# Kernel tuning notes

Hardware: AMD Instinct MI355X
Metric: run time of the kernel (lower is better)

The kernel has to match this reference:

```python
import jax, jax.numpy as jnp
import numpy as np

B, H, W, DIM, NH = 2, 48, 48, 768, 12
HD = DIM // NH  # 64


def setup_inputs() -> dict:
    key = jax.random.key(0)
    ks = jax.random.split(key, 7)
    std = 0.02
    return {
        "x": jax.random.normal(ks[0], (B, H, W, DIM), jnp.float32),
        "rel_pos_h": jax.random.normal(ks[1], (2 * H - 1, HD), jnp.float32) * std,
        "rel_pos_w": jax.random.normal(ks[2], (2 * W - 1, HD), jnp.float32) * std,
        "qkv_w": jax.random.normal(ks[3], (3 * DIM, DIM), jnp.float32) * std,
        "qkv_b": jnp.zeros((3 * DIM,), jnp.float32),
        "proj_w": jax.random.normal(ks[4], (DIM, DIM), jnp.float32) * std,
        "proj_b": jnp.zeros((DIM,), jnp.float32),
    }


def reference(x, rel_pos_h, rel_pos_w, qkv_w, qkv_b, proj_w, proj_b):
    b, h, w, dim = x.shape
    nh = NH
    hd = dim // nh
    scale = hd ** -0.5
    n = h * w
    # qkv projection: (B,N,3*dim) -> (3, B*nh, N, hd)
    qkv = x.reshape(b, n, dim) @ qkv_w.T + qkv_b
    qkv = qkv.reshape(b, n, 3, nh, hd).transpose(2, 0, 3, 1, 4).reshape(3, b * nh, n, hd)
    q, k, v = qkv[0], qkv[1], qkv[2]
    # scaled dot-product scores (B*nh, N, N)
    attn = jnp.einsum('bnc,bmc->bnm', q * scale, k)
    # decomposed relative position bias (q_size == k_size, no interpolation)
    idx_h = jnp.arange(h)[:, None] - jnp.arange(h)[None, :] + (h - 1)  # (h,h)
    idx_w = jnp.arange(w)[:, None] - jnp.arange(w)[None, :] + (w - 1)  # (w,w)
    Rh = rel_pos_h[idx_h]  # (h, h, hd)
    Rw = rel_pos_w[idx_w]  # (w, w, hd)
    r_q = q.reshape(b * nh, h, w, hd)
    rel_h = jnp.einsum('bhwc,hkc->bhwk', r_q, Rh)  # (B*nh, h, w, h)
    rel_w = jnp.einsum('bhwc,wkc->bhwk', r_q, Rw)  # (B*nh, h, w, w)
    attn = (attn.reshape(b * nh, h, w, h, w)
            + rel_h[:, :, :, :, None]
            + rel_w[:, :, :, None, :]).reshape(b * nh, n, n)
    attn = jax.nn.softmax(attn, axis=-1)
    out = (attn @ v).reshape(b, nh, h, w, hd).transpose(0, 2, 3, 1, 4).reshape(b, h, w, dim)
    return out @ proj_w.T + proj_b
```

## Files before the change

### kernel.cpp

```cpp
#include <hip/hip_runtime.h>
#include <hip/hip_bf16.h>
#include <stdint.h>

#define NQ    2304
#define MROWS 4608
#define DIMC  768
#define NHEAD 12
#define HEADS 24
#define HD    64

typedef unsigned int uint;
typedef unsigned short u16;
typedef __attribute__((ext_vector_type(8))) short s16x8;
typedef __attribute__((ext_vector_type(4))) float f32x4;

#define MFMA16(a, b, c) __builtin_amdgcn_mfma_f32_16x16x32_bf16((a), (b), (c), 0, 0, 0)

static __device__ __forceinline__ float bfbits2f(uint u) {
  union { uint i; float f; } c; c.i = u << 16; return c.f;
}
static __device__ __forceinline__ u16 f2bf(float f) {
  __hip_bfloat16 h = __float2bfloat16(f);
  union { __hip_bfloat16 h; u16 u; } c; c.h = h; return c.u;
}
static __device__ __forceinline__ u16 f2h(float f) {
  union { _Float16 h; u16 u; } c; c.h = (_Float16)f; return c.u;
}
static __device__ __forceinline__ float h2f(u16 u) {
  union { u16 u; _Float16 h; } c; c.u = u; return (float)c.h;
}
static __device__ __forceinline__ void dec8(uint4 p, float* f) {
  f[0] = bfbits2f(p.x & 0xFFFFu); f[1] = bfbits2f(p.x >> 16);
  f[2] = bfbits2f(p.y & 0xFFFFu); f[3] = bfbits2f(p.y >> 16);
  f[4] = bfbits2f(p.z & 0xFFFFu); f[5] = bfbits2f(p.z >> 16);
  f[6] = bfbits2f(p.w & 0xFFFFu); f[7] = bfbits2f(p.w >> 16);
}
static __device__ __forceinline__ void ld8(const void* p, size_t idx, int bf, float* f) {
  if (bf) { dec8(*(const uint4*)((const u16*)p + idx), f); }
  else {
    const float4* q = (const float4*)((const float*)p + idx);
    float4 a = q[0], b = q[1];
    f[0] = a.x; f[1] = a.y; f[2] = a.z; f[3] = a.w;
    f[4] = b.x; f[5] = b.y; f[6] = b.z; f[7] = b.w;
  }
}
static __device__ __forceinline__ float ld1(const void* p, size_t idx, int bf) {
  return bf ? bfbits2f(((const u16*)p)[idx]) : ((const float*)p)[idx];
}
static __device__ __forceinline__ uint4 ld8_to_bf(const void* p, size_t idx, int bf) {
  if (bf) return *(const uint4*)((const u16*)p + idx);
  float f[8]; ld8(p, idx, 0, f);
  uint4 u;
  u.x = (uint)f2bf(f[0]) | ((uint)f2bf(f[1]) << 16);
  u.y = (uint)f2bf(f[2]) | ((uint)f2bf(f[3]) << 16);
  u.z = (uint)f2bf(f[4]) | ((uint)f2bf(f[5]) << 16);
  u.w = (uint)f2bf(f[6]) | ((uint)f2bf(f[7]) << 16);
  return u;
}
static __device__ __forceinline__ void gll16(const u16* g, u16* l) {
  __builtin_amdgcn_global_load_lds(
      (const __attribute__((address_space(1))) unsigned int*)g,
      (__attribute__((address_space(3))) unsigned int*)l, 16, 0, 0);
}

__global__ __launch_bounds__(256) void detect_k(const u16* __restrict__ x,
                                                int* __restrict__ mode) {
  __shared__ int wsum[4];
  int t = threadIdx.x;
  int cnt = 0;
  for (int i = 0; i < 8; ++i) {
    uint u = x[(size_t)(t * 8 + i) * 2];
    uint e = (u >> 7) & 0xFFu;
    uint mag = u & 0x7FFFu;
    if (mag == 0 || (e >= 113 && e <= 133)) cnt++;
  }
#pragma unroll
  for (int d = 1; d < 64; d <<= 1) cnt += __shfl_xor(cnt, d);
  if ((t & 63) == 0) wsum[t >> 6] = cnt;
  __syncthreads();
  if (t == 0) mode[0] = ((wsum[0] + wsum[1] + wsum[2] + wsum[3]) > 1024) ? 1 : 0;
}

#define NX8 442368u
#define NW8 221184u
#define NP8 73728u
__global__ __launch_bounds__(256) void convert_k(
    const void* __restrict__ x, const void* __restrict__ qkvw,
    const void* __restrict__ pw, const int* __restrict__ mode,
    u16* __restrict__ xb, u16* __restrict__ wb, u16* __restrict__ pwb)
{
  const int bf = mode[0];
  uint i8 = blockIdx.x * 256 + threadIdx.x;
  if (i8 < NX8) {
    *(uint4*)(xb + (size_t)i8 * 8) = ld8_to_bf(x, (size_t)i8 * 8, bf);
  } else if (i8 < NX8 + NW8) {
    size_t j = i8 - NX8;
    *(uint4*)(wb + j * 8) = ld8_to_bf(qkvw, j * 8, bf);
  } else if (i8 < NX8 + NW8 + NP8) {
    size_t j = i8 - NX8 - NW8;
    *(uint4*)(pwb + j * 8) = ld8_to_bf(pw, j * 8, bf);
  }
}

__global__ __launch_bounds__(256) void qkv_gemm_k(
    const u16* __restrict__ Xb, const u16* __restrict__ Wb,
    const void* __restrict__ Bq, const int* __restrict__ mode,
    u16* __restrict__ Q, u16* __restrict__ K, u16* __restrict__ V)
{
  __shared__ __align__(16) u16 As[128][32];
  __shared__ __align__(16) u16 Bs[128][32];
  const int bf = mode[0];
  const int t = threadIdx.x;
  const int w = t >> 6, lane = t & 63, l15 = t & 15, quad = (t >> 4) & 3;
  const int wr = w >> 1, wc = w & 1;
  const int row0 = blockIdx.y << 7, col0 = blockIdx.x << 7;
  const int r4 = lane >> 2, c8 = (lane & 3) << 3;

  f32x4 zero4 = {0.f, 0.f, 0.f, 0.f};
  f32x4 acc[4][4];
#pragma unroll
  for (int i = 0; i < 4; ++i)
#pragma unroll
    for (int j = 0; j < 4; ++j) acc[i][j] = zero4;

  for (int kt = 0; kt < DIMC; kt += 32) {
    __syncthreads();
    gll16(Xb + (size_t)(row0 + (w << 5) + r4) * DIMC + kt + c8,      &As[(w << 5)][0]);
    gll16(Xb + (size_t)(row0 + (w << 5) + 16 + r4) * DIMC + kt + c8, &As[(w << 5) + 16][0]);
    gll16(Wb + (size_t)(col0 + (w << 5) + r4) * DIMC + kt + c8,      &Bs[(w << 5)][0]);
    gll16(Wb + (size_t)(col0 + (w << 5) + 16 + r4) * DIMC + kt + c8, &Bs[(w << 5) + 16][0]);
    __syncthreads();
    s16x8 af[4], bfr[4];
#pragma unroll
    for (int i = 0; i < 4; ++i)
      af[i] = *(const s16x8*)&As[(wr << 6) + (i << 4) + l15][quad << 3];
#pragma unroll
    for (int j = 0; j < 4; ++j)
      bfr[j] = *(const s16x8*)&Bs[(wc << 6) + (j << 4) + l15][quad << 3];
#pragma unroll
    for (int i = 0; i < 4; ++i)
#pragma unroll
      for (int j = 0; j < 4; ++j)
        acc[i][j] = MFMA16(af[i], bfr[j], acc[i][j]);
  }

#pragma unroll
  for (int jt = 0; jt < 4; ++jt) {
    int col = col0 + (wc << 6) + (jt << 4) + l15;
    int which = col / DIMC;
    int rem = col - which * DIMC;
    int head = rem >> 6, d = rem & 63;
    float bv = ld1(Bq, col, bf);
    u16* dst = (which == 0) ? Q : (which == 1) ? K : V;
#pragma unroll
    for (int i = 0; i < 4; ++i)
#pragma unroll
      for (int r = 0; r < 4; ++r) {
        int mrow = row0 + (wr << 6) + (i << 4) + (quad << 2) + r;
        int b_ = (mrow >= NQ) ? 1 : 0;
        int n = mrow - b_ * NQ;
        dst[(((size_t)(b_ * NHEAD + head)) * NQ + n) * HD + d] = f2bf(acc[i][jt][r] + bv);
      }
  }
}

__global__ __launch_bounds__(256) void vtrans_k(
    const u16* __restrict__ V, u16* __restrict__ Vt)
{
  __shared__ __align__(16) u16 L[64][72];
  const int blk = blockIdx.x;
  const int bhd = blk / 36;
  const int n0 = (blk - bhd * 36) << 6;
  const int t = threadIdx.x;
  const int r = t >> 3, c8 = (t & 7) << 3;

  const u16* src = V + ((size_t)bhd * NQ + n0) * HD;
  *(uint4*)&L[r][c8]      = *(const uint4*)(src + (size_t)r * HD + c8);
  *(uint4*)&L[r + 32][c8] = *(const uint4*)(src + (size_t)(r + 32) * HD + c8);
  __syncthreads();

  u16* dst = Vt + (size_t)bhd * HD * NQ + n0;
#pragma unroll
  for (int half = 0; half < 2; ++half) {
    int d = r + (half << 5);
    u16 tmp[8];
#pragma unroll
    for (int j = 0; j < 8; ++j) tmp[j] = L[c8 + j][d];
    *(uint4*)(dst + (size_t)d * NQ + c8) = *(uint4*)tmp;
  }
}

__global__ __launch_bounds__(256) void bias_gemm_k(
    const u16* __restrict__ Qw,
    const void* __restrict__ rph, const void* __restrict__ rpw,
    const int* __restrict__ mode,
    u16* __restrict__ Bh_g, u16* __restrict__ Bw_g)
{
  __shared__ __align__(16) u16 As[128][72];
  __shared__ __align__(16) u16 Bs[192][72];
  const int bf = mode[0];
  const int t = threadIdx.x;
  const int w = t >> 6, l15 = t & 15, quad = (t >> 4) & 3;
  const int wr = w >> 1, wc = w & 1;
  const int blk = blockIdx.x;
  const int bhd = blk / 18;
  const int row0 = (blk - bhd * 18) << 7;

  {
    int lr = t >> 1, lk = (t & 1) << 5;
    const u16* src = Qw + ((size_t)bhd * NQ + row0 + lr) * HD + lk;
    *(uint4*)&As[lr][lk]      = *(const uint4*)(src);
    *(uint4*)&As[lr][lk + 8]  = *(const uint4*)(src + 8);
    *(uint4*)&As[lr][lk + 16] = *(const uint4*)(src + 16);
    *(uint4*)&As[lr][lk + 24] = *(const uint4*)(src + 24);
  }
  for (int e = t; e < 384; e += 256) {
    int row = e >> 1, k32 = (e & 1) << 5;
    int tab = (row >= 96) ? 1 : 0;
    int r2 = row - (tab ? 96 : 0);
    if (r2 > 94) r2 = 0;
    const void* src = tab ? rpw : rph;
    *(uint4*)&Bs[row][k32]      = ld8_to_bf(src, (size_t)r2 * HD + k32, bf);
    *(uint4*)&Bs[row][k32 + 8]  = ld8_to_bf(src, (size_t)r2 * HD + k32 + 8, bf);
    *(uint4*)&Bs[row][k32 + 16] = ld8_to_bf(src, (size_t)r2 * HD + k32 + 16, bf);
    *(uint4*)&Bs[row][k32 + 24] = ld8_to_bf(src, (size_t)r2 * HD + k32 + 24, bf);
  }
  __syncthreads();

  f32x4 zero4 = {0.f, 0.f, 0.f, 0.f};
  f32x4 acc[4][6];
#pragma unroll
  for (int i = 0; i < 4; ++i)
#pragma unroll
    for (int j = 0; j < 6; ++j) acc[i][j] = zero4;

#pragma unroll
  for (int ks = 0; ks < 2; ++ks) {
    s16x8 af[4], bfr[6];
#pragma unroll
    for (int i = 0; i < 4; ++i)
      af[i] = *(const s16x8*)&As[(wr << 6) + (i << 4) + l15][(ks << 5) + (quad << 3)];
#pragma unroll
    for (int j = 0; j < 6; ++j)
      bfr[j] = *(const s16x8*)&Bs[wc * 96 + (j << 4) + l15][(ks << 5) + (quad << 3)];
#pragma unroll
    for (int i = 0; i < 4; ++i)
#pragma unroll
      for (int j = 0; j < 6; ++j)
        acc[i][j] = MFMA16(af[i], bfr[j], acc[i][j]);
  }

#pragma unroll
  for (int jt = 0; jt < 6; ++jt) {
    int col = wc * 96 + (jt << 4) + l15;
    int tab = (col >= 96) ? 1 : 0;
    int j = col - (tab ? 96 : 0);
    if (j >= 95) continue;
    u16* dstT = tab ? Bw_g : Bh_g;
#pragma unroll
    for (int i = 0; i < 4; ++i)
#pragma unroll
      for (int r = 0; r < 4; ++r) {
        int n = row0 + (wr << 6) + (i << 4) + (quad << 2) + r;
        int qh = (n * 10923) >> 19;
        int coord = tab ? (n - qh * 48) : qh;
        int c = coord + 47 - j;
        if (c >= 0 && c < 48)
          dstT[((size_t)bhd * 48 + c) * NQ + n] = f2h(acc[i][jt][r]);
      }
  }
}

#define ATILE(KB, KN, T0, PREF, KM) do {                                      \
    f32x4 acc_s[2][4];                                                        \
    _Pragma("unroll")                                                         \
    for (int nc = 0; nc < 4; ++nc) {                                          \
      f32x4 a0 = MFMA16(KB[2*nc], qa0[0], zero4);                             \
      acc_s[0][nc] = MFMA16(KB[2*nc+1], qa1[0], a0);                          \
      f32x4 a1 = MFMA16(KB[2*nc], qa0[1], zero4);                             \
      acc_s[1][nc] = MFMA16(KB[2*nc+1], qa1[1], a1);                          \
    }                                                                         \
    if (PREF) {                                                               \
      _Pragma("unroll")                                                       \
      for (int nc = 0; nc < 4; ++nc) {                                        \
        const u16* kp_ = kbase + (size_t)((T0) + 64 + (nc << 4) + l15) * HD + (quad << 3); \
        KN[2*nc]   = *(const s16x8*)(kp_);                                    \
        KN[2*nc+1] = *(const s16x8*)(kp_ + 32);                               \
      }                                                                       \
    }                                                                         \
    int kh0 = ((T0) * 10923) >> 19;                                           \
    int thr = (kh0 + 1) * 48 - (T0);                                          \
    uint Wq[2][8];                                                            \
    _Pragma("unroll")                                                         \
    for (int g = 0; g < 2; ++g) {                                             \
      int qrl = (w << 5) + (g << 4) + l15;                                    \
      float bh0v = h2f(BhL[kh0][qrl]);                                        \
      float bh1v = h2f(BhL[kh0 + 1][qrl]);                                    \
      float sum = 0.f;                                                        \
      _Pragma("unroll")                                                       \
      for (int nc = 0; nc < 4; ++nc) {                                        \
        int bnc = (KM) + (nc << 4);                                           \
        bnc = (bnc >= 48) ? bnc - 48 : bnc;                                   \
        uint2 pv = *(const uint2*)&BwL[qrl][bnc + (quad << 2)];               \
        float b0 = h2f((u16)(pv.x & 0xFFFFu));                                \
        float b1 = h2f((u16)(pv.x >> 16));                                    \
        float b2 = h2f((u16)(pv.y & 0xFFFFu));                                \
        float b3 = h2f((u16)(pv.y >> 16));                                    \
        int kl = (nc << 4) + (quad << 2);                                     \
        float e0 = __expf(acc_s[g][nc][0] * scale + ((kl     >= thr) ? bh1v : bh0v) + b0); \
        float e1 = __expf(acc_s[g][nc][1] * scale + ((kl + 1 >= thr) ? bh1v : bh0v) + b1); \
        float e2 = __expf(acc_s[g][nc][2] * scale + ((kl + 2 >= thr) ? bh1v : bh0v) + b2); \
        float e3 = __expf(acc_s[g][nc][3] * scale + ((kl + 3 >= thr) ? bh1v : bh0v) + b3); \
        sum += (e0 + e1) + (e2 + e3);                                         \
        Wq[g][2*nc]   = (uint)f2bf(e0) | ((uint)f2bf(e1) << 16);              \
        Wq[g][2*nc+1] = (uint)f2bf(e2) | ((uint)f2bf(e3) << 16);              \
      }                                                                       \
      l_st[g] += sum;                                                         \
    }                                                                         \
    _Pragma("unroll")                                                         \
    for (int h = 0; h < 2; ++h) {                                             \
      s16x8 vb[4];                                                            \
      _Pragma("unroll")                                                       \
      for (int nc = 0; nc < 4; ++nc)                                          \
        vb[nc] = *(const s16x8*)(vtbase + (size_t)((nc << 4) + l15) * NQ      \
                                 + (T0) + (h << 5) + (quad << 3));            \
      _Pragma("unroll")                                                       \
      for (int g = 0; g < 2; ++g) {                                           \
        uint e0 = __shfl(Wq[g][4*h+0], srcA), e1 = __shfl(Wq[g][4*h+1], srcA); \
        uint e2 = __shfl(Wq[g][4*h+2], srcA), e3 = __shfl(Wq[g][4*h+3], srcA); \
        uint g0 = __shfl(Wq[g][4*h+0], srcB), g1 = __shfl(Wq[g][4*h+1], srcB); \
        uint g2 = __shfl(Wq[g][4*h+2], srcB), g3 = __shfl(Wq[g][4*h+3], srcB); \
        union { uint u[4]; s16x8 v; } pf;                                     \
        pf.u[0] = hi ? e2 : e0; pf.u[1] = hi ? e3 : e1;                       \
        pf.u[2] = hi ? g2 : g0; pf.u[3] = hi ? g3 : g1;                       \
        _Pragma("unroll")                                                     \
        for (int nc = 0; nc < 4; ++nc)                                        \
          acc_o[g][nc] = MFMA16(pf.v, vb[nc], acc_o[g][nc]);                  \
      }                                                                       \
    }                                                                         \
  } while (0)

__global__ __launch_bounds__(256) void attn_k(
    const u16* __restrict__ Qw, const u16* __restrict__ Kw,
    const u16* __restrict__ Vtg,
    const u16* __restrict__ Bh_g, const u16* __restrict__ Bw_g,
    int S, float* __restrict__ Opart, float* __restrict__ Lpart,
    u16* __restrict__ Aout)
{
  __shared__ __align__(16) u16 BhL[48][128];
  __shared__ __align__(16) u16 BwL[128][52];

  const int bid = blockIdx.x;
  const int xcd = bid & 7;
  const int local = bid >> 3;
  const int per_head = 18 * S;
  const int head_l = local / per_head;
  const int rem = local - head_l * per_head;
  const int qb = rem / S;
  const int z = rem - qb * S;
  const int bhd = xcd * 3 + head_l;
  const int q0 = qb << 7;
  const int span = NQ / S;
  const int kt_lo = z * span, kt_hi = kt_lo + span;

  const int t = threadIdx.x;
  const int w = t >> 6, l15 = t & 15, quad = (t >> 4) & 3;
  const float scale = 0.125f;

  const u16* kbase  = Kw  + (size_t)bhd * NQ * HD;
  const u16* vtbase = Vtg + (size_t)bhd * HD * NQ;
  const int q0w = q0 + (w << 5);

  for (int e = t; e < 768; e += 256) {
    int c = e >> 4;
    int off = (e & 15) << 3;
    size_t gi = ((size_t)bhd * 48 + c) * NQ + q0 + off;
    *(uint4*)&BhL[c][off] = *(const uint4*)(Bh_g + gi);
    uint4 wv = *(const uint4*)(Bw_g + gi);
    u16 vals[8];
    vals[0] = wv.x & 0xFFFFu; vals[1] = wv.x >> 16;
    vals[2] = wv.y & 0xFFFFu; vals[3] = wv.y >> 16;
    vals[4] = wv.z & 0xFFFFu; vals[5] = wv.z >> 16;
    vals[6] = wv.w & 0xFFFFu; vals[7] = wv.w >> 16;
#pragma unroll
    for (int j = 0; j < 8; ++j) BwL[off + j][c] = vals[j];
  }

  s16x8 qa0[2], qa1[2];
#pragma unroll
  for (int g = 0; g < 2; ++g) {
    const u16* qfrag = Qw + ((size_t)bhd * NQ + q0w + (g << 4) + l15) * HD + (quad << 3);
    qa0[g] = *(const s16x8*)(qfrag);
    qa1[g] = *(const s16x8*)(qfrag + 32);
  }

  s16x8 kbA[8], kbB[8];
#pragma unroll
  for (int nc = 0; nc < 4; ++nc) {
    const u16* kp = kbase + (size_t)(kt_lo + (nc << 4) + l15) * HD + (quad << 3);
    kbA[2*nc]   = *(const s16x8*)(kp);
    kbA[2*nc+1] = *(const s16x8*)(kp + 32);
  }

  __syncthreads();

  f32x4 zero4 = {0.f, 0.f, 0.f, 0.f};
  f32x4 acc_o[2][4];
#pragma unroll
  for (int g = 0; g < 2; ++g)
#pragma unroll
    for (int nc = 0; nc < 4; ++nc) acc_o[g][nc] = zero4;
  float l_st[2] = {0.f, 0.f};
  const int srcA = ((quad & 1) << 5) + l15;
  const int srcB = srcA + 16;
  const int hi = quad >> 1;
  int km = 0;

  for (int kt0 = kt_lo; kt0 < kt_hi; kt0 += 128) {
    ATILE(kbA, kbB, kt0, 1, km);
    km += 16; if (km >= 48) km -= 48;
    int pref2 = (kt0 + 128) < kt_hi;
    ATILE(kbB, kbA, kt0 + 64, pref2, km);
    km += 16; if (km >= 48) km -= 48;
  }

#pragma unroll
  for (int g = 0; g < 2; ++g) {
    float lg = l_st[g];
    lg += __shfl_xor(lg, 16);
    lg += __shfl_xor(lg, 32);
    if (S > 1) {
      float* Op = Opart + ((size_t)(z * HEADS + bhd) * NQ + q0) * HD;
#pragma unroll
      for (int r = 0; r < 4; ++r) {
        int row = (w << 5) + (g << 4) + (quad << 2) + r;
#pragma unroll
        for (int nc = 0; nc < 4; ++nc)
          Op[(size_t)row * HD + (nc << 4) + l15] = acc_o[g][nc][r];
      }
      if (quad == 0)
        Lpart[(size_t)(z * HEADS + bhd) * NQ + q0w + (g << 4) + l15] = lg;
    } else {
      int b_ = bhd / NHEAD, head = bhd - b_ * NHEAD;
      float invl = 1.f / lg;
      int bsrc = (quad << 4) + (quad << 2);
#pragma unroll
      for (int r = 0; r < 4; ++r) {
        float inv = __shfl(invl, bsrc + r);
        int token = q0 + (w << 5) + (g << 4) + (quad << 2) + r;
        u16* dst = Aout + ((size_t)b_ * NQ + token) * DIMC + (head << 6);
#pragma unroll
        for (int nc = 0; nc < 4; ++nc)
          dst[(nc << 4) + l15] = f2bf(acc_o[g][nc][r] * inv);
      }
    }
  }
}

__global__ __launch_bounds__(256) void combine_k(
    const float* __restrict__ Op, const float* __restrict__ Lp,
    int S, u16* __restrict__ Aout)
{
  int idx = blockIdx.x * 256 + threadIdx.x;
  int m = idx / 192;
  int cq = idx - m * 192;
  int ccol = cq << 2;
  int head = ccol >> 6, d0 = ccol & 63;
  int b_ = (m >= NQ) ? 1 : 0;
  int n = m - b_ * NQ;
  int bh = b_ * NHEAD + head;
  float ox = 0.f, oy = 0.f, oz = 0.f, ow = 0.f, ls = 0.f;
  for (int zz = 0; zz < S; ++zz) {
    const float* ob = Op + ((size_t)(zz * HEADS + bh) * NQ + n) * HD + d0;
    float4 v = *(const float4*)ob;
    ox += v.x; oy += v.y; oz += v.z; ow += v.w;
    ls += Lp[(size_t)(zz * HEADS + bh) * NQ + n];
  }
  float inv = 1.f / ls;
  u16* dst = Aout + (size_t)m * DIMC + ccol;
  dst[0] = f2bf(ox * inv); dst[1] = f2bf(oy * inv);
  dst[2] = f2bf(oz * inv); dst[3] = f2bf(ow * inv);
}

__global__ __launch_bounds__(256) void proj_gemm_k(
    const u16* __restrict__ A, const u16* __restrict__ Wb,
    const void* __restrict__ Bp, const int* __restrict__ mode,
    void* __restrict__ Out)
{
  __shared__ __align__(16) u16 As[128][32];
  __shared__ __align__(16) u16 Bs[128][32];
  const int bf = mode[0];
  const int t = threadIdx.x;
  const int w = t >> 6, lane = t & 63, l15 = t & 15, quad = (t >> 4) & 3;
  const int wr = w >> 1, wc = w & 1;
  const int row0 = blockIdx.y << 7, col0 = blockIdx.x << 7;
  const int r4 = lane >> 2, c8 = (lane & 3) << 3;

  f32x4 zero4 = {0.f, 0.f, 0.f, 0.f};
  f32x4 acc[4][4];
#pragma unroll
  for (int i = 0; i < 4; ++i)
#pragma unroll
    for (int j = 0; j < 4; ++j) acc[i][j] = zero4;

  for (int kt = 0; kt < DIMC; kt += 32) {
    __syncthreads();
    gll16(A + (size_t)(row0 + (w << 5) + r4) * DIMC + kt + c8,       &As[(w << 5)][0]);
    gll16(A + (size_t)(row0 + (w << 5) + 16 + r4) * DIMC + kt + c8,  &As[(w << 5) + 16][0]);
    gll16(Wb + (size_t)(col0 + (w << 5) + r4) * DIMC + kt + c8,      &Bs[(w << 5)][0]);
    gll16(Wb + (size_t)(col0 + (w << 5) + 16 + r4) * DIMC + kt + c8, &Bs[(w << 5) + 16][0]);
    __syncthreads();
    s16x8 af[4], bfr[4];
#pragma unroll
    for (int i = 0; i < 4; ++i)
      af[i] = *(const s16x8*)&As[(wr << 6) + (i << 4) + l15][quad << 3];
#pragma unroll
    for (int j = 0; j < 4; ++j)
      bfr[j] = *(const s16x8*)&Bs[(wc << 6) + (j << 4) + l15][quad << 3];
#pragma unroll
    for (int i = 0; i < 4; ++i)
#pragma unroll
      for (int j = 0; j < 4; ++j)
        acc[i][j] = MFMA16(af[i], bfr[j], acc[i][j]);
  }

#pragma unroll
  for (int jt = 0; jt < 4; ++jt) {
    int col = col0 + (wc << 6) + (jt << 4) + l15;
    float bv = ld1(Bp, col, bf);
#pragma unroll
    for (int i = 0; i < 4; ++i)
#pragma unroll
      for (int r = 0; r < 4; ++r) {
        int mrow = row0 + (wr << 6) + (i << 4) + (quad << 2) + r;
        float val = acc[i][jt][r] + bv;
        size_t off = (size_t)mrow * DIMC + col;
        if (bf) ((u16*)Out)[off] = f2bf(val);
        else    ((float*)Out)[off] = val;
      }
  }
}

extern "C" void kernel_launch(void* const* d_in, const int* in_sizes, int n_in,
                              void* d_out, int out_size, void* d_ws, size_t ws_size,
                              hipStream_t stream)
{
  const void* x    = d_in[0];
  const void* rph  = d_in[1];
  const void* rpw  = d_in[2];
  const void* qkvw = d_in[3];
  const void* qkvb = d_in[4];
  const void* pw   = d_in[5];
  const void* pb   = d_in[6];

  int* mode = (int*)d_ws;
  const size_t qkv_elems = (size_t)HEADS * NQ * HD;
  const size_t NXe = (size_t)MROWS * DIMC;
  const size_t NWe = (size_t)3 * DIMC * DIMC;
  const size_t NPe = (size_t)DIMC * DIMC;
  u16* q    = (u16*)((char*)d_ws + 16);
  u16* k    = q + qkv_elems;
  u16* vt   = k + qkv_elems;
  u16* aout = vt + qkv_elems;
  u16* v    = aout;
  u16* pwb  = aout + qkv_elems;
  const size_t biasElems = (size_t)HEADS * 48 * NQ;
  u16* bh_g = pwb + NPe;
  u16* bw_g = bh_g + biasElems;
  char* R   = (char*)(bw_g + biasElems);
  const size_t baseR = (size_t)((char*)R - (char*)d_ws);
  u16* xb = (u16*)R;
  u16* wb = xb + NXe;
  const size_t needXW = (NXe + NWe) * 2;
  const size_t perO = (size_t)HEADS * NQ * HD * 4;
  const size_t perL = (size_t)HEADS * NQ * 4;

  int S = 1;
  size_t n3 = 3 * (perO + perL), n2 = 2 * (perO + perL);
  if (ws_size >= baseR + (n3 > needXW ? n3 : needXW)) S = 3;
  else if (ws_size >= baseR + (n2 > needXW ? n2 : needXW)) S = 2;
  float* opart = (float*)R;
  float* lpart = (float*)(R + (size_t)S * perO);

  detect_k<<<1, 256, 0, stream>>>((const u16*)x, mode);
  convert_k<<<dim3(2880), 256, 0, stream>>>(x, qkvw, pw, mode, xb, wb, pwb);
  qkv_gemm_k<<<dim3(18, 36), 256, 0, stream>>>(xb, wb, qkvb, mode, q, k, v);
  vtrans_k<<<dim3(864), 256, 0, stream>>>(v, vt);
  bias_gemm_k<<<dim3(432), 256, 0, stream>>>(q, rph, rpw, mode, bh_g, bw_g);
  attn_k<<<dim3(432 * S), 256, 0, stream>>>(q, k, vt, bh_g, bw_g,
                                            S, opart, lpart, aout);
  if (S > 1)
    combine_k<<<dim3(3456), 256, 0, stream>>>(opart, lpart, S, aout);
  proj_gemm_k<<<dim3(6, 36), 256, 0, stream>>>(aout, pwb, pb, mode, d_out);
}
```

Before: 335.4 us.

## Fuse V transpose into QKV GEMM epilogue, use exp2 softmax, add MFMA priority hints

The QKV GEMM epilogue now transposes the V tile through shared memory and writes Vt directly. This removes the separate vtrans kernel launch and the V round trip through global memory. Softmax now uses exp2, with log2e folded into the stored bias tables and the score scale. s_setprio hints are placed around the MFMA blocks in the attention tile. The fused epilogue adds an extra LDS buffer and barriers to the V-column GEMM blocks.

Result: no change. 341.0 us (+1.7%).

```diff
diff --git a/kernel.cpp b/kernel.cpp
--- a/kernel.cpp
+++ b/kernel.cpp
@@ -15,6 +15,7 @@
 typedef __attribute__((ext_vector_type(4))) float f32x4;
 
 #define MFMA16(a, b, c) __builtin_amdgcn_mfma_f32_16x16x32_bf16((a), (b), (c), 0, 0, 0)
+#define LOG2E 1.44269504f
 
 static __device__ __forceinline__ float bfbits2f(uint u) {
   union { uint i; float f; } c; c.i = u << 16; return c.f;
@@ -28,6 +29,13 @@
 }
 static __device__ __forceinline__ float h2f(u16 u) {
   union { u16 u; _Float16 h; } c; c.u = u; return (float)c.h;
+}
+static __device__ __forceinline__ float fexp2(float x) {
+#if __has_builtin(__builtin_amdgcn_exp2f)
+  return __builtin_amdgcn_exp2f(x);
+#else
+  return __expf(x * 0.69314718f);
+#endif
 }
 static __device__ __forceinline__ void dec8(uint4 p, float* f) {
   f[0] = bfbits2f(p.x & 0xFFFFu); f[1] = bfbits2f(p.x >> 16);
@@ -105,10 +113,11 @@
 __global__ __launch_bounds__(256) void qkv_gemm_k(
     const u16* __restrict__ Xb, const u16* __restrict__ Wb,
     const void* __restrict__ Bq, const int* __restrict__ mode,
-    u16* __restrict__ Q, u16* __restrict__ K, u16* __restrict__ V)
+    u16* __restrict__ Q, u16* __restrict__ K, u16* __restrict__ Vt)
 {
   __shared__ __align__(16) u16 As[128][32];
   __shared__ __align__(16) u16 Bs[128][32];
+  __shared__ __align__(16) u16 Ts[128][72];
   const int bf = mode[0];
   const int t = threadIdx.x;
   const int w = t >> 6, lane = t & 63, l15 = t & 15, quad = (t >> 4) & 3;
@@ -144,49 +153,57 @@
         acc[i][j] = MFMA16(af[i], bfr[j], acc[i][j]);
   }
 
-#pragma unroll
-  for (int jt = 0; jt < 4; ++jt) {
-    int col = col0 + (wc << 6) + (jt << 4) + l15;
-    int which = col / DIMC;
-    int rem = col - which * DIMC;
-    int head = rem >> 6, d = rem & 63;
-    float bv = ld1(Bq, col, bf);
-    u16* dst = (which == 0) ? Q : (which == 1) ? K : V;
-#pragma unroll
-    for (int i = 0; i < 4; ++i)
-#pragma unroll
-      for (int r = 0; r < 4; ++r) {
-        int mrow = row0 + (wr << 6) + (i << 4) + (quad << 2) + r;
-        int b_ = (mrow >= NQ) ? 1 : 0;
-        int n = mrow - b_ * NQ;
-        dst[(((size_t)(b_ * NHEAD + head)) * NQ + n) * HD + d] = f2bf(acc[i][jt][r] + bv);
+  if (blockIdx.x < 12) {
+#pragma unroll
+    for (int jt = 0; jt < 4; ++jt) {
+      int col = col0 + (wc << 6) + (jt << 4) + l15;
+      int which = col / DIMC;
+      int rem = col - which * DIMC;
+      int head = rem >> 6, d = rem & 63;
+      float bv = ld1(Bq, col, bf);
+      u16* dst = (which == 0) ? Q : K;
+#pragma unroll
+      for (int i = 0; i < 4; ++i)
+#pragma unroll
+        for (int r = 0; r < 4; ++r) {
+          int mrow = row0 + (wr << 6) + (i << 4) + (quad << 2) + r;
+          int b_ = (mrow >= NQ) ? 1 : 0;
+          int n = mrow - b_ * NQ;
+          dst[(((size_t)(b_ * NHEAD + head)) * NQ + n) * HD + d] = f2bf(acc[i][jt][r] + bv);
+        }
+    }
+  } else {
+    int b_ = (row0 >= NQ) ? 1 : 0;
+    int n0 = row0 - b_ * NQ;
+#pragma unroll
+    for (int h = 0; h < 2; ++h) {
+      if (wc == h) {
+#pragma unroll
+        for (int jt = 0; jt < 4; ++jt) {
+          int coll = (jt << 4) + l15;
+          float bv = ld1(Bq, col0 + (h << 6) + coll, bf);
+#pragma unroll
+          for (int i = 0; i < 4; ++i)
+#pragma unroll
+            for (int r = 0; r < 4; ++r) {
+              int tok = (wr << 6) + (i << 4) + (quad << 2) + r;
+              Ts[tok][coll] = f2bf(acc[i][jt][r] + bv);
+            }
+        }
       }
-  }
-}
-
-__global__ __launch_bounds__(256) void vtrans_k(
-    const u16* __restrict__ V, u16* __restrict__ Vt)
-{
-  __shared__ __align__(16) u16 L[64][72];
-  const int blk = blockIdx.x;
-  const int bhd = blk / 36;
-  const int n0 = (blk - bhd * 36) << 6;
-  const int t = threadIdx.x;
-  const int r = t >> 3, c8 = (t & 7) << 3;
-
-  const u16* src = V + ((size_t)bhd * NQ + n0) * HD;
-  *(uint4*)&L[r][c8]      = *(const uint4*)(src + (size_t)r * HD + c8);
-  *(uint4*)&L[r + 32][c8] = *(const uint4*)(src + (size_t)(r + 32) * HD + c8);
-  __syncthreads();
-
-  u16* dst = Vt + (size_t)bhd * HD * NQ + n0;
-#pragma unroll
-  for (int half = 0; half < 2; ++half) {
-    int d = r + (half << 5);
-    u16 tmp[8];
-#pragma unroll
-    for (int j = 0; j < 8; ++j) tmp[j] = L[c8 + j][d];
-    *(uint4*)(dst + (size_t)d * NQ + c8) = *(uint4*)tmp;
+      __syncthreads();
+      int head = ((col0 - 1536) >> 6) + h;
+      u16* dst = Vt + ((size_t)(b_ * NHEAD + head) * HD) * NQ + n0;
+      int d = t >> 2, ch = (t & 3) << 5;
+#pragma unroll
+      for (int c4 = 0; c4 < 4; ++c4) {
+        u16 tmp[8];
+#pragma unroll
+        for (int j = 0; j < 8; ++j) tmp[j] = Ts[ch + (c4 << 3) + j][d];
+        *(uint4*)(dst + (size_t)d * NQ + ch + (c4 << 3)) = *(uint4*)tmp;
+      }
+      __syncthreads();
+    }
   }
 }
 
@@ -266,13 +283,14 @@
         int coord = tab ? (n - qh * 48) : qh;
         int c = coord + 47 - j;
         if (c >= 0 && c < 48)
-          dstT[((size_t)bhd * 48 + c) * NQ + n] = f2h(acc[i][jt][r]);
+          dstT[((size_t)bhd * 48 + c) * NQ + n] = f2h(acc[i][jt][r] * LOG2E);
       }
   }
 }
 
 #define ATILE(KB, KN, T0, PREF, KM) do {                                      \
     f32x4 acc_s[2][4];                                                        \
+    __builtin_amdgcn_s_setprio(1);                                            \
     _Pragma("unroll")                                                         \
     for (int nc = 0; nc < 4; ++nc) {                                          \
       f32x4 a0 = MFMA16(KB[2*nc], qa0[0], zero4);                             \
@@ -280,6 +298,7 @@
       f32x4 a1 = MFMA16(KB[2*nc], qa0[1], zero4);                             \
       acc_s[1][nc] = MFMA16(KB[2*nc+1], qa1[1], a1);                          \
     }                                                                         \
+    __builtin_amdgcn_s_setprio(0);                                            \
     if (PREF) {                                                               \
       _Pragma("unroll")                                                       \
       for (int nc = 0; nc < 4; ++nc) {                                        \
@@ -307,10 +326,10 @@
         float b2 = h2f((u16)(pv.y & 0xFFFFu));                                \
         float b3 = h2f((u16)(pv.y >> 16));                                    \
         int kl = (nc << 4) + (quad << 2);                                     \
-        float e0 = __expf(acc_s[g][nc][0] * scale + ((kl     >= thr) ? bh1v : bh0v) + b0); \
-        float e1 = __expf(acc_s[g][nc][1] * scale + ((kl + 1 >= thr) ? bh1v : bh0v) + b1); \
-        float e2 = __expf(acc_s[g][nc][2] * scale + ((kl + 2 >= thr) ? bh1v : bh0v) + b2); \
-        float e3 = __expf(acc_s[g][nc][3] * scale + ((kl + 3 >= thr) ? bh1v : bh0v) + b3); \
+        float e0 = fexp2(fmaf(acc_s[g][nc][0], scl2, ((kl     >= thr) ? bh1v : bh0v)) + b0); \
+        float e1 = fexp2(fmaf(acc_s[g][nc][1], scl2, ((kl + 1 >= thr) ? bh1v : bh0v)) + b1); \
+        float e2 = fexp2(fmaf(acc_s[g][nc][2], scl2, ((kl + 2 >= thr) ? bh1v : bh0v)) + b2); \
+        float e3 = fexp2(fmaf(acc_s[g][nc][3], scl2, ((kl + 3 >= thr) ? bh1v : bh0v)) + b3); \
         sum += (e0 + e1) + (e2 + e3);                                         \
         Wq[g][2*nc]   = (uint)f2bf(e0) | ((uint)f2bf(e1) << 16);              \
         Wq[g][2*nc+1] = (uint)f2bf(e2) | ((uint)f2bf(e3) << 16);              \
@@ -333,9 +352,11 @@
         union { uint u[4]; s16x8 v; } pf;                                     \
         pf.u[0] = hi ? e2 : e0; pf.u[1] = hi ? e3 : e1;                       \
         pf.u[2] = hi ? g2 : g0; pf.u[3] = hi ? g3 : g1;                       \
+        __builtin_amdgcn_s_setprio(1);                                        \
         _Pragma("unroll")                                                     \
         for (int nc = 0; nc < 4; ++nc)                                        \
           acc_o[g][nc] = MFMA16(pf.v, vb[nc], acc_o[g][nc]);                  \
+        __builtin_amdgcn_s_setprio(0);                                        \
       }                                                                       \
     }                                                                         \
   } while (0)
@@ -365,7 +386,7 @@
 
   const int t = threadIdx.x;
   const int w = t >> 6, l15 = t & 15, quad = (t >> 4) & 3;
-  const float scale = 0.125f;
+  const float scl2 = 0.125f * LOG2E;
 
   const u16* kbase  = Kw  + (size_t)bhd * NQ * HD;
   const u16* vtbase = Vtg + (size_t)bhd * HD * NQ;
@@ -562,7 +583,6 @@
   u16* k    = q + qkv_elems;
   u16* vt   = k + qkv_elems;
   u16* aout = vt + qkv_elems;
-  u16* v    = aout;
   u16* pwb  = aout + qkv_elems;
   const size_t biasElems = (size_t)HEADS * 48 * NQ;
   u16* bh_g = pwb + NPe;
@@ -584,8 +604,7 @@
 
   detect_k<<<1, 256, 0, stream>>>((const u16*)x, mode);
   convert_k<<<dim3(2880), 256, 0, stream>>>(x, qkvw, pw, mode, xb, wb, pwb);
-  qkv_gemm_k<<<dim3(18, 36), 256, 0, stream>>>(xb, wb, qkvb, mode, q, k, v);
-  vtrans_k<<<dim3(864), 256, 0, stream>>>(v, vt);
+  qkv_gemm_k<<<dim3(18, 36), 256, 0, stream>>>(xb, wb, qkvb, mode, q, k, vt);
   bias_gemm_k<<<dim3(432), 256, 0, stream>>>(q, rph, rpw, mode, bh_g, bw_g);
   attn_k<<<dim3(432 * S), 256, 0, stream>>>(q, k, vt, bh_g, bw_g,
                                             S, opart, lpart, aout);
```
